# Kernel tuning notes

Measured on AMD Instinct MI355X. Metric: run time of the kernel, lower is better.

Reference implementation:

```python
import jax, jax.numpy as jnp
import numpy as np

DIM = 512
H = 8
HD = DIM // H
MAXREL = 8
BF16_MIN = -3.3895313892515355e38  # torch.finfo(torch.bfloat16).min


def setup_inputs() -> dict:
    key = jax.random.key(0)
    k1, k2, k3, k4, k5, k6 = jax.random.split(key, 6)
    b, l, n, d = 4, 16, 64, DIM
    x = jax.random.normal(k1, (b, l, n, d), dtype=jnp.float32)
    time_embeddings = jax.random.normal(k2, (b, l, d), dtype=jnp.float32)
    # relative frame positions in [-MAXREL, MAXREL]
    pos = jax.random.randint(k3, (b, l, l), 0, 2 * MAXREL + 1) - MAXREL
    pos = pos.astype(jnp.int64) if jax.config.read('jax_enable_x64') else pos.astype(jnp.int32)
    # causal mask over frames
    mask = jnp.tril(jnp.ones((l, l), dtype=jnp.int32))[None].repeat(b, axis=0)
    # params (torch Linear convention: out = x @ W.T)
    W_qkv = jax.random.normal(k4, (3 * d, d), dtype=jnp.float32) * (1.0 / np.sqrt(d))
    W_tqkv = jax.random.normal(k5, (3 * HD, d), dtype=jnp.float32) * (1.0 / np.sqrt(d))
    # xavier_uniform for embeddings table [2*max+1, head_dim]
    lim = np.sqrt(6.0 / (2 * MAXREL + 1 + HD))
    emb_table = jax.random.uniform(k6, (2 * MAXREL + 1, HD), minval=-lim, maxval=lim, dtype=jnp.float32)
    return {"x": x, "time_embeddings": time_embeddings, "pos": pos, "mask": mask,
            "W_qkv": W_qkv, "W_tqkv": W_tqkv, "emb_table": emb_table}


def _forward(x, time_embeddings, pos, mask, W_qkv, W_tqkv, emb_table):
    b, l, n, d = x.shape
    h, hd = H, HD
    N = l * n
    scale = np.sqrt(d).astype(np.float32)

    qkv = jnp.einsum('blnd,ed->blne', x, W_qkv)
    q, k, v = jnp.split(qkv, 3, axis=-1)

    def to_heads(t):  # [b,l,n,d] -> [b,h,l,n,hd]
        return t.reshape(b, l, n, h, hd).transpose(0, 3, 1, 2, 4)
    q, k, v = to_heads(q), to_heads(k), to_heads(v)

    # time qkv: [b,l,3*hd] -> broadcast add over heads and tokens
    tqkv = jnp.einsum('bld,ed->ble', time_embeddings, W_tqkv)
    qt, kt, vt = jnp.split(tqkv, 3, axis=-1)  # each [b,l,hd]

    def add_t(t, tt):  # tt: [b,l,hd] -> [b,1,l,1,hd]
        return t + tt[:, None, :, None, :]
    q = add_t(q, qt).reshape(b, h, N, hd)
    k = add_t(k, kt).reshape(b, h, N, hd)
    v = add_t(v, vt).reshape(b, h, N, hd)

    # content scores [b,h,N,N]
    qk = jnp.einsum('bhqd,bhkd->bhqk', q, k)

    # relative position bias
    idx = jnp.clip(pos, -MAXREL, MAXREL) + MAXREL          # [b,l,l]
    emb = emb_table[idx]                                    # [b,l,l,hd]
    # q chunked: [b,h,(l n),hd] -> [b,h,n,l,hd] (l is major in (l n))
    qc = q.reshape(b, h, l, n, hd).transpose(0, 1, 3, 2, 4)
    qr = jnp.einsum('bhnqd,bqkd->bhqnk', qc, emb)           # [b,h,l,n,l]
    qr = jnp.broadcast_to(qr[..., None], (b, h, l, n, l, n)).reshape(b, h, N, N)

    attn = (qk + qr) / scale

    # expand frame mask [b,l,l] -> [b,N,N]
    exp_mask = jnp.broadcast_to(mask[:, :, None, :, None], (b, l, n, l, n)).reshape(b, N, N)
    attn = jnp.where(exp_mask[:, None] == 0, BF16_MIN, attn)

    attn = jax.nn.softmax(attn, axis=-1)
    out = jnp.einsum('bhqk,bhkd->bhqd', attn, v)            # [b,h,N,hd]
    out = out.reshape(b, h, l, n, hd).transpose(0, 2, 3, 1, 4).reshape(b, l, n, d)
    return out


def reference(x, time_embeddings, pos, mask, W_qkv, W_tqkv, emb_table):
    return _forward(x, time_embeddings, pos, mask, W_qkv, W_tqkv, emb_table)
```

## Files before the change

kernel.cpp:

```cpp
#include <hip/hip_runtime.h>

typedef unsigned short u16;
typedef __attribute__((ext_vector_type(8))) short short8;
typedef __attribute__((ext_vector_type(4))) float f32x4;
typedef __attribute__((ext_vector_type(4))) u16 u16x4;

#define BB 4
#define LL 16
#define DD 512
#define NH 8
#define HDIM 64
#define NSEQ 1024
#define E3 1536
#define INV_SCALE 0.04419417382415922f

__device__ __forceinline__ u16 f2bf(float f) {
  union { float f; unsigned u; } v; v.f = f;
  unsigned u = v.u;
  unsigned r = u + 0x7fffu + ((u >> 16) & 1u);
  return (u16)(r >> 16);
}

__device__ __forceinline__ unsigned cvtpk(float lo, float hi) {
  unsigned r;
  asm("v_cvt_pk_bf16_f32 %0, %1, %2" : "=v"(r) : "v"(lo), "v"(hi));
  return r;
}

__device__ __forceinline__ uint4 pack8(float4 a, float4 b) {
  uint4 r;
  r.x = (unsigned)f2bf(a.x) | ((unsigned)f2bf(a.y) << 16);
  r.y = (unsigned)f2bf(a.z) | ((unsigned)f2bf(a.w) << 16);
  r.z = (unsigned)f2bf(b.x) | ((unsigned)f2bf(b.y) << 16);
  r.w = (unsigned)f2bf(b.z) | ((unsigned)f2bf(b.w) << 16);
  return r;
}

__device__ __forceinline__ void stage16(const u16* g, u16* l) {
  __builtin_amdgcn_global_load_lds((const __attribute__((address_space(1))) unsigned int*)g,
                                   (__attribute__((address_space(3))) unsigned int*)l,
                                   16, 0, 0);
}

__global__ __launch_bounds__(256) void prep_convert(const float* __restrict__ x,
                                                    const float* __restrict__ w,
                                                    u16* __restrict__ xbf,
                                                    u16* __restrict__ wbf) {
  const int nx = (4096 * DD) / 4;
  const int nw = (E3 * DD) / 4;
  int i = blockIdx.x * 256 + threadIdx.x;
  const float4* src;
  uint2* dst;
  int j;
  if (i < nx) { src = (const float4*)x; dst = (uint2*)xbf; j = i; }
  else if (i < nx + nw) { src = (const float4*)w; dst = (uint2*)wbf; j = i - nx; }
  else return;
  float4 v = src[j];
  unsigned lo = (unsigned)f2bf(v.x) | ((unsigned)f2bf(v.y) << 16);
  unsigned hi = (unsigned)f2bf(v.z) | ((unsigned)f2bf(v.w) << 16);
  dst[j] = make_uint2(lo, hi);
}

__global__ __launch_bounds__(256) void tproj_mfma(const float* __restrict__ te,
                                                  const float* __restrict__ wt,
                                                  float* __restrict__ tq) {
  __shared__ u16 At[64][72];
  __shared__ u16 Bt[64][72];
  int bn = blockIdx.x;
  int tid = threadIdx.x;
  int w = tid >> 6, l = tid & 63;
  int l15 = l & 15, l16 = l >> 4;
  int r0 = tid >> 3, c0 = (tid & 7) * 8;
  f32x4 acc[4] = {};
  for (int kt = 0; kt < DD; kt += 64) {
    {
      const float* ta = &te[(size_t)r0 * DD + kt + c0];
      const float* tb = &te[(size_t)(r0 + 32) * DD + kt + c0];
      *(uint4*)&At[r0][c0]      = pack8(*(const float4*)ta, *(const float4*)(ta + 4));
      *(uint4*)&At[r0 + 32][c0] = pack8(*(const float4*)tb, *(const float4*)(tb + 4));
      const float* wa = &wt[(size_t)(bn * 64 + r0) * DD + kt + c0];
      const float* wb_ = &wt[(size_t)(bn * 64 + r0 + 32) * DD + kt + c0];
      *(uint4*)&Bt[r0][c0]      = pack8(*(const float4*)wa, *(const float4*)(wa + 4));
      *(uint4*)&Bt[r0 + 32][c0] = pack8(*(const float4*)wb_, *(const float4*)(wb_ + 4));
    }
    __syncthreads();
#pragma unroll
    for (int ks = 0; ks < 2; ++ks) {
      short8 bfr = *(const short8*)&Bt[w * 16 + l15][ks * 32 + l16 * 8];
#pragma unroll
      for (int mt = 0; mt < 4; ++mt) {
        short8 afr = *(const short8*)&At[mt * 16 + l15][ks * 32 + l16 * 8];
        acc[mt] = __builtin_amdgcn_mfma_f32_16x16x32_bf16(afr, bfr, acc[mt], 0, 0, 0);
      }
    }
    __syncthreads();
  }
  int e = bn * 64 + w * 16 + l15;
#pragma unroll
  for (int mt = 0; mt < 4; ++mt)
#pragma unroll
    for (int r = 0; r < 4; ++r)
      tq[(mt * 16 + l16 * 4 + r) * 192 + e] = acc[mt][r];
}

__global__ __launch_bounds__(256) void gemm_qkv(const u16* __restrict__ xb,
                                                const u16* __restrict__ wb,
                                                const float* __restrict__ tq,
                                                u16* __restrict__ qp,
                                                u16* __restrict__ kp,
                                                u16* __restrict__ vt) {
  __shared__ u16 As[2][128][72];
  __shared__ u16 Bs[2][128][72];
  int bn = blockIdx.x;
  int bm = blockIdx.y;
  int tid = threadIdx.x;
  int w = tid >> 6, l = tid & 63;
  int wr = w >> 1, wc = w & 1;
  int l15 = l & 15, l16 = l >> 4;
  int r0 = tid >> 3, c0 = (tid & 7) * 8;

  f32x4 acc[4][4] = {};
  uint4 ra[4], rb[4];

#define LOADT(kt)                                                                    \
  {                                                                                  \
    _Pragma("unroll") for (int c = 0; c < 4; ++c) {                                  \
      ra[c] = *(const uint4*)&xb[(size_t)(bm * 128 + c * 32 + r0) * DD + (kt) + c0]; \
      rb[c] = *(const uint4*)&wb[(size_t)(bn * 128 + c * 32 + r0) * DD + (kt) + c0]; \
    }                                                                                \
  }
#define STORET(buf)                                                                  \
  {                                                                                  \
    _Pragma("unroll") for (int c = 0; c < 4; ++c) {                                  \
      *(uint4*)&As[buf][c * 32 + r0][c0] = ra[c];                                    \
      *(uint4*)&Bs[buf][c * 32 + r0][c0] = rb[c];                                    \
    }                                                                                \
  }

  LOADT(0);
  STORET(0);
  __syncthreads();
  int cur = 0;
#pragma unroll
  for (int i = 0; i < 8; ++i) {
    if (i < 7) LOADT((i + 1) * 64);
#pragma unroll
    for (int ks = 0; ks < 2; ++ks) {
      short8 af[4], bf[4];
#pragma unroll
      for (int mt = 0; mt < 4; ++mt)
        af[mt] = *(const short8*)&As[cur][wr * 64 + mt * 16 + l15][ks * 32 + l16 * 8];
#pragma unroll
      for (int nt = 0; nt < 4; ++nt)
        bf[nt] = *(const short8*)&Bs[cur][wc * 64 + nt * 16 + l15][ks * 32 + l16 * 8];
#pragma unroll
      for (int mt = 0; mt < 4; ++mt)
#pragma unroll
        for (int nt = 0; nt < 4; ++nt)
          acc[mt][nt] = __builtin_amdgcn_mfma_f32_16x16x32_bf16(af[mt], bf[nt], acc[mt][nt], 0, 0, 0);
    }
    if (i < 7) STORET(cur ^ 1);
    __syncthreads();
    cur ^= 1;
  }
#undef LOADT
#undef STORET

  int part = bn >> 2;
#pragma unroll
  for (int mt = 0; mt < 4; ++mt) {
    int m0 = bm * 128 + wr * 64 + mt * 16 + l16 * 4;
    int b = m0 >> 10;
    int li = (m0 >> 6) & 15;
    int nn0 = m0 & 1023;
    const float* tqrow = &tq[(b * LL + li) * 192 + part * 64];
#pragma unroll
    for (int nt = 0; nt < 4; ++nt) {
      int din = (bn & 3) * 128 + wc * 64 + nt * 16 + l15;
      int hh = din >> 6, hd = din & 63;
      float t = tqrow[hd];
      size_t bh = (size_t)(b * NH + hh);
      if (part == 2) {
        u16x4 pk;
#pragma unroll
        for (int r = 0; r < 4; ++r) pk[r] = f2bf(acc[mt][nt][r] + t);
        *(u16x4*)&vt[(bh * HDIM + hd) * NSEQ + nn0] = pk;
      } else {
        u16* dst = (part == 0) ? qp : kp;
#pragma unroll
        for (int r = 0; r < 4; ++r)
          dst[(bh * NSEQ + nn0 + r) * HDIM + hd] = f2bf(acc[mt][nt][r] + t);
      }
    }
  }
}

__global__ __launch_bounds__(256, 2) void attn_kernel(const u16* __restrict__ qp,
                                                      const u16* __restrict__ kp,
                                                      const u16* __restrict__ vt,
                                                      const int* __restrict__ pos,
                                                      const float* __restrict__ emb,
                                                      float* __restrict__ out) {
  __shared__ __align__(16) u16 Kt[2][64][64];
  __shared__ __align__(16) u16 Vt[2][64][64];
  __shared__ __align__(16) float Ot[4][16][68];

  int blk = blockIdx.x;
  int bhid = blk & 31;
  int qf = 15 - (blk >> 5);
  int b = bhid >> 3, h = bhid & 7;
  int tid = threadIdx.x;
  int rg = tid >> 6;
  int l = tid & 63;
  int l15 = l & 15, l16 = l >> 4;
  int srow = l >> 3, c8 = l & 7;
  int schunk = c8 ^ srow;
  int swzA = (l15 & 7) << 4;

  size_t bh = (size_t)(b * NH + h);
  const u16* Kb = kp + bh * NSEQ * HDIM;
  const u16* Vb = vt + bh * HDIM * NSEQ;
  int rowl0 = rg * 16 + srow;
  int rowl1 = rowl0 + 8;

#define STAGE(kf_, buf_)                                                   \
  {                                                                        \
    stage16(Kb + ((kf_) * 64 + rowl0) * HDIM + schunk * 8,                 \
            &Kt[buf_][rg * 16 + 0][0] + l * 8);                            \
    stage16(Kb + ((kf_) * 64 + rowl1) * HDIM + schunk * 8,                 \
            &Kt[buf_][rg * 16 + 8][0] + l * 8);                            \
    stage16(Vb + (size_t)rowl0 * NSEQ + (kf_) * 64 + schunk * 8,           \
            &Vt[buf_][rg * 16 + 0][0] + l * 8);                            \
    stage16(Vb + (size_t)rowl1 * NSEQ + (kf_) * 64 + schunk * 8,           \
            &Vt[buf_][rg * 16 + 8][0] + l * 8);                            \
  }

  const u16* Qg = qp + (bh * NSEQ + qf * 64 + rg * 16) * HDIM;
  short8 aq[2];
  aq[0] = *(const short8*)&Qg[l15 * HDIM + l16 * 8];
  aq[1] = *(const short8*)&Qg[l15 * HDIM + 32 + l16 * 8];

  STAGE(0, 0);
  if (qf > 0) STAGE(1, 1);

  int pp = pos[(b * LL + qf) * LL + l15];
  pp = (pp < -8 ? -8 : (pp > 8 ? 8 : pp)) + 8;
  const float* ev = emb + pp * HDIM;
  f32x4 bfragT = {};
#pragma unroll
  for (int ks = 0; ks < 2; ++ks) {
    float4 e0 = *(const float4*)&ev[ks * 32 + l16 * 8];
    float4 e1 = *(const float4*)&ev[ks * 32 + l16 * 8 + 4];
    short8 ef;
    ef[0] = (short)f2bf(e0.x); ef[1] = (short)f2bf(e0.y);
    ef[2] = (short)f2bf(e0.z); ef[3] = (short)f2bf(e0.w);
    ef[4] = (short)f2bf(e1.x); ef[5] = (short)f2bf(e1.y);
    ef[6] = (short)f2bf(e1.z); ef[7] = (short)f2bf(e1.w);
    bfragT = __builtin_amdgcn_mfma_f32_16x16x32_bf16(ef, aq[ks], bfragT, 0, 0, 0);
  }

  f32x4 o[4] = {};
  float lsum = 0.f;

  if (qf > 0) { asm volatile("s_waitcnt vmcnt(4)" ::: "memory"); }
  else        { asm volatile("s_waitcnt vmcnt(0)" ::: "memory"); }
  __syncthreads();

  for (int kf = 0; kf <= qf; ++kf) {
    int cur = kf & 1;
    const char* ktb = (const char*)&Kt[cur][0][0];
    const char* vtb = (const char*)&Vt[cur][0][0];

    f32x4 s[4] = {};
    __builtin_amdgcn_s_setprio(1);
#pragma unroll
    for (int ks = 0; ks < 2; ++ks)
#pragma unroll
      for (int nt = 0; nt < 4; ++nt) {
        short8 kfrag = *(const short8*)(ktb + (nt * 16 + l15) * 128 + ((ks * 64 + l16 * 16) ^ swzA));
        s[nt] = __builtin_amdgcn_mfma_f32_16x16x32_bf16(kfrag, aq[ks], s[nt], 0, 0, 0);
      }
    __builtin_amdgcn_s_setprio(0);

    float bb = __shfl(bfragT[kf & 3], ((kf >> 2) << 4) | l15) * INV_SCALE;

    float pv[4][4];
#pragma unroll
    for (int nt = 0; nt < 4; ++nt)
#pragma unroll
      for (int r = 0; r < 4; ++r) {
        float p = __expf(fmaf(s[nt][r], INV_SCALE, bb));
        pv[nt][r] = p;
        lsum += p;
      }

#pragma unroll
    for (int w32 = 0; w32 < 2; ++w32) {
      union { unsigned u[4]; short8 s8; } pf;
      pf.u[0] = cvtpk(pv[w32 * 2][0], pv[w32 * 2][1]);
      pf.u[1] = cvtpk(pv[w32 * 2][2], pv[w32 * 2][3]);
      pf.u[2] = cvtpk(pv[w32 * 2 + 1][0], pv[w32 * 2 + 1][1]);
      pf.u[3] = cvtpk(pv[w32 * 2 + 1][2], pv[w32 * 2 + 1][3]);
      int off0 = w32 * 64 + l16 * 8;
      int cp = off0 & ~15, sub = off0 & 15;
      __builtin_amdgcn_s_setprio(1);
#pragma unroll
      for (int dt = 0; dt < 4; ++dt) {
        int d = dt * 16 + l15;
        int sx = (d & 7) << 4;
        union { uint2 h2[2]; short8 s8; } vf;
        vf.h2[0] = *(const uint2*)(vtb + d * 128 + (cp ^ sx) + sub);
        vf.h2[1] = *(const uint2*)(vtb + d * 128 + ((cp + 32) ^ sx) + sub);
        o[dt] = __builtin_amdgcn_mfma_f32_16x16x32_bf16(vf.s8, pf.s8, o[dt], 0, 0, 0);
      }
      __builtin_amdgcn_s_setprio(0);
    }

    if (kf < qf) {
      __syncthreads();
      if (kf + 2 <= qf) {
        STAGE(kf + 2, cur);
        asm volatile("s_waitcnt vmcnt(4)" ::: "memory");
      } else {
        asm volatile("s_waitcnt vmcnt(0)" ::: "memory");
      }
      __syncthreads();
    }
  }
#undef STAGE

  lsum += __shfl_xor(lsum, 16);
  lsum += __shfl_xor(lsum, 32);
  float inv = 1.0f / lsum;

#pragma unroll
  for (int dt = 0; dt < 4; ++dt)
#pragma unroll
    for (int r = 0; r < 4; ++r)
      Ot[rg][l15][dt * 16 + l16 * 4 + r] = o[dt][r] * inv;

  float* outp = out + ((size_t)(b * LL + qf) * 64 + rg * 16) * DD + h * 64;
#pragma unroll
  for (int rr = 0; rr < 4; ++rr) {
    int q = rr * 4 + l16;
    float4 v = *(const float4*)&Ot[rg][q][l15 * 4];
    *(float4*)&outp[(size_t)q * DD + l15 * 4] = v;
  }
}

extern "C" void kernel_launch(void* const* d_in, const int* in_sizes, int n_in,
                              void* d_out, int out_size, void* d_ws, size_t ws_size,
                              hipStream_t stream) {
  const float* x    = (const float*)d_in[0];
  const float* te   = (const float*)d_in[1];
  const int*   pos  = (const int*)d_in[2];
  const float* wqkv = (const float*)d_in[4];
  const float* wt   = (const float*)d_in[5];
  const float* emb  = (const float*)d_in[6];
  float* out = (float*)d_out;
  char* ws = (char*)d_ws;

  const size_t OFF_XBF = 0;
  const size_t OFF_WBF  = OFF_XBF + (size_t)4096 * DD * 2;
  const size_t OFF_TQ   = OFF_WBF + (size_t)E3 * DD * 2;
  const size_t OFF_QKV  = OFF_TQ + (size_t)64 * 192 * 4;
  const size_t PLANE = (size_t)BB * NH * NSEQ * HDIM;

  u16*   xbf  = (u16*)(ws + OFF_XBF);
  u16*   wbf  = (u16*)(ws + OFF_WBF);
  float* tq   = (float*)(ws + OFF_TQ);
  u16*   qpl  = (u16*)(ws + OFF_QKV);
  u16*   kpl  = qpl + PLANE;
  u16*   vtl  = qpl + 2 * PLANE;

  prep_convert<<<2816, 256, 0, stream>>>(x, wqkv, xbf, wbf);
  tproj_mfma<<<3, 256, 0, stream>>>(te, wt, tq);
  gemm_qkv<<<dim3(12, 32), 256, 0, stream>>>(xbf, wbf, tq, qpl, kpl, vtl);
  attn_kernel<<<512, 256, 0, stream>>>(qpl, kpl, vtl, pos, emb, out);
}
```

Baseline: 122.2 us.

## Split attention blocks into two 128-thread halves and write output directly

Each attention block now covers 32 query rows with two waves instead of 64 rows with four, so the grid doubles to 1024 blocks. Every wave stages twice as many K/V rows, with the vmcnt waits adjusted to match. The LDS transpose buffer for the output is removed and results go straight to global memory as float4 stores. This is meant to give more blocks for load balance and occupancy across the causal triangle. In exchange, each K/V tile is loaded from global memory twice, and the direct stores are less coalesced.

```diff
diff --git a/kernel.cpp b/kernel.cpp
--- a/kernel.cpp
+++ b/kernel.cpp
@@ -195,7 +195,7 @@
   }
 }
 
-__global__ __launch_bounds__(256, 2) void attn_kernel(const u16* __restrict__ qp,
+__global__ __launch_bounds__(128, 2) void attn_kernel(const u16* __restrict__ qp,
                                                       const u16* __restrict__ kp,
                                                       const u16* __restrict__ vt,
                                                       const int* __restrict__ pos,
@@ -203,11 +203,11 @@
                                                       float* __restrict__ out) {
   __shared__ __align__(16) u16 Kt[2][64][64];
   __shared__ __align__(16) u16 Vt[2][64][64];
-  __shared__ __align__(16) float Ot[4][16][68];
 
   int blk = blockIdx.x;
-  int bhid = blk & 31;
-  int qf = 15 - (blk >> 5);
+  int qf = 15 - (blk >> 6);
+  int bhid = (blk >> 1) & 31;
+  int half = blk & 1;
   int b = bhid >> 3, h = bhid & 7;
   int tid = threadIdx.x;
   int rg = tid >> 6;
@@ -216,6 +216,7 @@
   int srow = l >> 3, c8 = l & 7;
   int schunk = c8 ^ srow;
   int swzA = (l15 & 7) << 4;
+  int rga = half * 2 + rg;
 
   size_t bh = (size_t)(b * NH + h);
   const u16* Kb = kp + bh * NSEQ * HDIM;
@@ -223,19 +224,27 @@
   int rowl0 = rg * 16 + srow;
   int rowl1 = rowl0 + 8;
 
-#define STAGE(kf_, buf_)                                                   \
-  {                                                                        \
-    stage16(Kb + ((kf_) * 64 + rowl0) * HDIM + schunk * 8,                 \
-            &Kt[buf_][rg * 16 + 0][0] + l * 8);                            \
-    stage16(Kb + ((kf_) * 64 + rowl1) * HDIM + schunk * 8,                 \
-            &Kt[buf_][rg * 16 + 8][0] + l * 8);                            \
-    stage16(Vb + (size_t)rowl0 * NSEQ + (kf_) * 64 + schunk * 8,           \
-            &Vt[buf_][rg * 16 + 0][0] + l * 8);                            \
-    stage16(Vb + (size_t)rowl1 * NSEQ + (kf_) * 64 + schunk * 8,           \
-            &Vt[buf_][rg * 16 + 8][0] + l * 8);                            \
-  }
-
-  const u16* Qg = qp + (bh * NSEQ + qf * 64 + rg * 16) * HDIM;
+#define STAGE(kf_, buf_)                                                       \
+  {                                                                            \
+    stage16(Kb + ((kf_) * 64 + rowl0) * HDIM + schunk * 8,                     \
+            &Kt[buf_][rg * 16 + 0][0] + l * 8);                                \
+    stage16(Kb + ((kf_) * 64 + rowl1) * HDIM + schunk * 8,                     \
+            &Kt[buf_][rg * 16 + 8][0] + l * 8);                                \
+    stage16(Kb + ((kf_) * 64 + rowl0 + 32) * HDIM + schunk * 8,                \
+            &Kt[buf_][rg * 16 + 32][0] + l * 8);                               \
+    stage16(Kb + ((kf_) * 64 + rowl1 + 32) * HDIM + schunk * 8,                \
+            &Kt[buf_][rg * 16 + 40][0] + l * 8);                               \
+    stage16(Vb + (size_t)rowl0 * NSEQ + (kf_) * 64 + schunk * 8,               \
+            &Vt[buf_][rg * 16 + 0][0] + l * 8);                                \
+    stage16(Vb + (size_t)rowl1 * NSEQ + (kf_) * 64 + schunk * 8,               \
+            &Vt[buf_][rg * 16 + 8][0] + l * 8);                                \
+    stage16(Vb + (size_t)(rowl0 + 32) * NSEQ + (kf_) * 64 + schunk * 8,        \
+            &Vt[buf_][rg * 16 + 32][0] + l * 8);                               \
+    stage16(Vb + (size_t)(rowl1 + 32) * NSEQ + (kf_) * 64 + schunk * 8,        \
+            &Vt[buf_][rg * 16 + 40][0] + l * 8);                               \
+  }
+
+  const u16* Qg = qp + (bh * NSEQ + qf * 64 + rga * 16) * HDIM;
   short8 aq[2];
   aq[0] = *(const short8*)&Qg[l15 * HDIM + l16 * 8];
   aq[1] = *(const short8*)&Qg[l15 * HDIM + 32 + l16 * 8];
@@ -262,7 +271,7 @@
   f32x4 o[4] = {};
   float lsum = 0.f;
 
-  if (qf > 0) { asm volatile("s_waitcnt vmcnt(4)" ::: "memory"); }
+  if (qf > 0) { asm volatile("s_waitcnt vmcnt(8)" ::: "memory"); }
   else        { asm volatile("s_waitcnt vmcnt(0)" ::: "memory"); }
   __syncthreads();
 
@@ -320,7 +329,7 @@
       __syncthreads();
       if (kf + 2 <= qf) {
         STAGE(kf + 2, cur);
-        asm volatile("s_waitcnt vmcnt(4)" ::: "memory");
+        asm volatile("s_waitcnt vmcnt(8)" ::: "memory");
       } else {
         asm volatile("s_waitcnt vmcnt(0)" ::: "memory");
       }
@@ -333,18 +342,13 @@
   lsum += __shfl_xor(lsum, 32);
   float inv = 1.0f / lsum;
 
-#pragma unroll
-  for (int dt = 0; dt < 4; ++dt)
-#pragma unroll
-    for (int r = 0; r < 4; ++r)
-      Ot[rg][l15][dt * 16 + l16 * 4 + r] = o[dt][r] * inv;
-
-  float* outp = out + ((size_t)(b * LL + qf) * 64 + rg * 16) * DD + h * 64;
-#pragma unroll
-  for (int rr = 0; rr < 4; ++rr) {
-    int q = rr * 4 + l16;
-    float4 v = *(const float4*)&Ot[rg][q][l15 * 4];
-    *(float4*)&outp[(size_t)q * DD + l15 * 4] = v;
+  float* outp = out + ((size_t)(b * LL + qf) * 64 + rga * 16) * DD + h * 64;
+#pragma unroll
+  for (int dt = 0; dt < 4; ++dt) {
+    float4 v;
+    v.x = o[dt][0] * inv; v.y = o[dt][1] * inv;
+    v.z = o[dt][2] * inv; v.w = o[dt][3] * inv;
+    *(float4*)&outp[(size_t)l15 * DD + dt * 16 + l16 * 4] = v;
   }
 }
 
@@ -376,5 +380,5 @@
   prep_convert<<<2816, 256, 0, stream>>>(x, wqkv, xbf, wbf);
   tproj_mfma<<<3, 256, 0, stream>>>(te, wt, tq);
   gemm_qkv<<<dim3(12, 32), 256, 0, stream>>>(xbf, wbf, tq, qpl, kpl, vtl);
-  attn_kernel<<<512, 256, 0, stream>>>(qpl, kpl, vtl, pos, emb, out);
-}
+  attn_kernel<<<1024, 128, 0, stream>>>(qpl, kpl, vtl, pos, emb, out);
+}
```

Measured after the change: 120.4 us. About the same (-1.5%).
